# Kernel tuning notes

Hardware: AMD Instinct MI355X
Metric: run time of the kernel (lower is better)

## Reference

```python
import jax, jax.numpy as jnp
import numpy as np

H, C, D = 8, 32, 128  # num_heads, att_head_size, inp_dim
LN_EPS = 1e-5


def setup_inputs() -> dict:
    key = jax.random.key(0)
    ks = jax.random.split(key, 12)
    B, I, L = 1, 128, 256
    z_ij = jax.random.normal(ks[0], (B, I, L, D), dtype=jnp.float32)
    d_jk = jax.random.uniform(ks[1], (B, L, L, 1), dtype=jnp.float32)
    mask_z = jnp.ones((B, I, L), dtype=jnp.float32)
    s = 0.05
    return {
        "z_ij": z_ij,
        "d_jk": d_jk,
        "mask_z": mask_z,
        "ln_gamma": jnp.ones((D,), jnp.float32),
        "ln_beta": jnp.zeros((D,), jnp.float32),
        "Wq": jax.random.normal(ks[2], (D, H * C), jnp.float32) * s,
        "Wk": jax.random.normal(ks[3], (D, H * C), jnp.float32) * s,
        "Wv": jax.random.normal(ks[4], (D, H * C), jnp.float32) * s,
        "Wb": jax.random.normal(ks[5], (D, H), jnp.float32) * s,
        "Wd": jax.random.normal(ks[6], (1, H), jnp.float32) * s,
        "Wg": jax.random.normal(ks[7], (D, H * C), jnp.float32) * s,
        "bg": jnp.zeros((H * C,), jnp.float32),
        "Wf": jax.random.normal(ks[8], (H * C, D), jnp.float32) * s,
        "bf": jnp.zeros((D,), jnp.float32),
    }


def reference(z_ij, d_jk, mask_z, ln_gamma, ln_beta, Wq, Wk, Wv, Wb, Wd, Wg, bg, Wf, bf):
    B, I, L, _ = z_ij.shape
    # LayerNorm over last dim
    mu = jnp.mean(z_ij, axis=-1, keepdims=True)
    var = jnp.mean(jnp.square(z_ij - mu), axis=-1, keepdims=True)
    z = (z_ij - mu) * jax.lax.rsqrt(var + LN_EPS) * ln_gamma + ln_beta

    rs = lambda x: x.reshape(x.shape[:-1] + (H, C))  # [..., H*C] -> [..., H, C]
    q = rs(z @ Wq) * (H ** -0.5)                  # [B,I,L,H,C]
    k = rs(z @ Wk)                                # [B,I,L,H,C]
    v = rs(z @ Wv)                                # [B,I,L,H,C]

    b = jnp.transpose(z @ Wb, (0, 1, 3, 2))[..., None]       # [B,I,H,Q,1]
    d = jnp.transpose(d_jk @ Wd, (0, 3, 1, 2))[:, None]      # [B,1,H,Q,K]

    logits = jnp.einsum('biqhc,bikhc->bihqk', q, k) + b + d  # [B,I,H,Q,K]
    att_mask = 1e9 * (mask_z[:, :, None, None, :] - 1.0)
    logits = logits + att_mask
    weights = jax.nn.softmax(logits, axis=-1)

    weighted = jnp.einsum('bihqk,bikhc->biqhc', weights, v)  # [B,I,Q,H,C]
    g = jax.nn.sigmoid(rs(z @ Wg + bg))                      # [B,I,Q,H,C]
    out = (g * weighted).reshape(B, I, L, H * C)
    out = out @ Wf + bf
    out = out * mask_z[..., None]
    return out
```

## Files before the change

kernel.cpp:

```cpp
#include <hip/hip_runtime.h>
#include <hip/hip_bf16.h>
#include <math.h>

#define HH 8
#define CC 32
#define DD 128
#define HC 256
#define II 128
#define LL 256
#define NROW (II*LL)
#define LN_EPS 1e-5f

typedef float f32x4 __attribute__((ext_vector_type(4)));
typedef short short8 __attribute__((ext_vector_type(8)));
typedef short short4v __attribute__((ext_vector_type(4)));
typedef unsigned short us;

static __device__ __forceinline__ us bfc(float x) {
    return __builtin_bit_cast(us, __float2bfloat16(x));
}
static __device__ __forceinline__ float bf2f(us h) {
    return __builtin_bit_cast(float, ((unsigned int)h) << 16);
}

__global__ __launch_bounds__(256) void k_ln(const float* __restrict__ z,
                                            const float* __restrict__ gamma,
                                            const float* __restrict__ beta,
                                            us* __restrict__ zn)
{
    const int t = threadIdx.x;
    const int row = blockIdx.x * 4 + (t >> 6);
    const int lane = t & 63;
    float2 x = *(const float2*)(z + (size_t)row * DD + lane * 2);
    float s = x.x + x.y;
    float s2 = x.x * x.x + x.y * x.y;
#pragma unroll
    for (int off = 1; off < 64; off <<= 1) {
        s  += __shfl_xor(s, off, 64);
        s2 += __shfl_xor(s2, off, 64);
    }
    float mu = s * (1.0f / DD);
    float var = s2 * (1.0f / DD) - mu * mu;
    float rstd = rsqrtf(var + LN_EPS);
    float2 gm = *(const float2*)(gamma + lane * 2);
    float2 bt = *(const float2*)(beta + lane * 2);
    float y0 = (x.x - mu) * rstd * gm.x + bt.x;
    float y1 = (x.y - mu) * rstd * gm.y + bt.y;
    unsigned int pk = (unsigned int)bfc(y0) | ((unsigned int)bfc(y1) << 16);
    ((unsigned int*)zn)[(size_t)row * 64 + lane] = pk;
}

__global__ __launch_bounds__(256) void k_wprep(const float* __restrict__ Wq,
                                               const float* __restrict__ Wk,
                                               const float* __restrict__ Wv,
                                               const float* __restrict__ Wg,
                                               const float* __restrict__ Wf,
                                               us* __restrict__ F,
                                               us* __restrict__ WfpH,
                                               us* __restrict__ WfpL)
{
    const int bid = blockIdx.x;
    if (bid < 128) {
        const int mat = bid >> 5;
        const float* W = (mat == 0) ? Wq : (mat == 1) ? Wk : (mat == 2) ? Wv : Wg;
        const float scale = (mat == 0) ? 0.35355339059327373f : 1.0f;
        int base = (bid & 31) * 1024 + threadIdx.x * 4;
        float4 wv = *(const float4*)(W + base);
        int k = base >> 8, n0 = base & 255;
        int ks = k >> 5, kk = k & 31;
        int slot = ((kk >> 4) << 2) | (kk & 3);
        int gg = (kk >> 2) & 3;
        float vals[4] = {wv.x, wv.y, wv.z, wv.w};
        us* Fb = F + mat * 32768;
#pragma unroll
        for (int e = 0; e < 4; ++e) {
            int n = n0 + e;
            int lane = (n & 15) | (gg << 4);
            Fb[((size_t)(ks * 16 + (n >> 4)) * 64 + lane) * 8 + slot] = bfc(vals[e] * scale);
        }
    } else {
        int idx = ((bid - 128) * 256 + threadIdx.x) * 4;
#pragma unroll
        for (int e = 0; e < 4; ++e, ++idx) {
            int k = idx >> 7, n = idx & 127;
            float w = Wf[idx];
            us hi = bfc(w);
            us lo = bfc(w - bf2f(hi));
            int kk = k & 31;
            int g = (kk >> 2) & 3, b = kk >> 4, j0 = kk & 3;
            int lane = (n & 15) | (g << 4);
            size_t dst = ((size_t)((k >> 5) * 8 + (n >> 4)) * 64 + lane) * 8 + b * 4 + j0;
            WfpH[dst] = hi;
            WfpL[dst] = lo;
        }
    }
}

__global__ __launch_bounds__(256, 4) void k_proj(const us* __restrict__ zn,
                                                 const us* __restrict__ F,
                                                 const float* __restrict__ bg,
                                                 us* __restrict__ Qf,
                                                 us* __restrict__ Kf,
                                                 us* __restrict__ Vtf,
                                                 us* __restrict__ Pg)
{
    const int rb = blockIdx.x, cb = blockIdx.y, t = threadIdx.x;
    const int m0 = rb * 128, n0 = cb * 128;
    const int mat = n0 >> 8, lc0 = n0 & 255;
    __shared__ us A[128][136];

#pragma unroll
    for (int e = 0; e < 8; ++e) {
        int cid = e * 256 + t;
        int row = cid >> 4, c = cid & 15;
        uint4 q = *(const uint4*)(zn + (size_t)(m0 + row) * DD + c * 8);
        int ks = c >> 2, cc = c & 3;
        int fe = (cc & 1) * 16 + (cc >> 1) * 4;
        *(uint2*)&A[row][ks * 32 + fe]     = make_uint2(q.x, q.y);
        *(uint2*)&A[row][ks * 32 + fe + 8] = make_uint2(q.z, q.w);
    }
    __syncthreads();

    const int lane = t & 63, w = t >> 6;
    const int wm = w & 1, wn = w >> 1;
    const int l0 = lane & 15, g = lane >> 4;
    const us* Fb = F + mat * 32768 + ((size_t)((lc0 >> 4) + wn * 4) * 64 + lane) * 8;
    f32x4 acc[4][4];
#pragma unroll
    for (int a = 0; a < 4; ++a)
#pragma unroll
        for (int b = 0; b < 4; ++b) acc[a][b] = (f32x4){0, 0, 0, 0};

#pragma unroll
    for (int ks = 0; ks < 4; ++ks) {
        short8 af[4], bfr[4];
#pragma unroll
        for (int mf = 0; mf < 4; ++mf)
            af[mf] = *(const short8*)&A[wm * 64 + mf * 16 + l0][ks * 32 + 8 * g];
#pragma unroll
        for (int nf = 0; nf < 4; ++nf)
            bfr[nf] = *(const short8*)(Fb + (size_t)(ks * 16 + nf) * 512);
#pragma unroll
        for (int mf = 0; mf < 4; ++mf)
#pragma unroll
            for (int nf = 0; nf < 4; ++nf)
                acc[mf][nf] = __builtin_amdgcn_mfma_f32_16x16x32_bf16(af[mf], bfr[nf], acc[mf][nf], 0, 0, 0);
    }

    __syncthreads();
    us (*Cs)[136] = A;
#pragma unroll
    for (int nf = 0; nf < 4; ++nf) {
        int lcol = wn * 64 + nf * 16 + l0;
        float bgv = (mat == 3) ? bg[lc0 + lcol] : 0.0f;
#pragma unroll
        for (int mf = 0; mf < 4; ++mf) {
#pragma unroll
            for (int r = 0; r < 4; ++r) {
                float v = acc[mf][nf][r];
                if (mat == 3) v = 1.0f / (1.0f + __expf(-(v + bgv)));
                Cs[wm * 64 + mf * 16 + 4 * g + r][lcol] = bfc(v);
            }
        }
    }
    __syncthreads();

    const int i = m0 >> 8, half = (m0 >> 7) & 1;
    if (mat <= 1) {
        us* Dst = (mat == 0) ? Qf : Kf;
#pragma unroll
        for (int e = 0; e < 8; ++e) {
            int sub = e * 256 + t;
            int lane2 = sub & 63;
            int l0b = lane2 & 15, gb = lane2 >> 4;
            int rest = sub >> 6;
            int hl = rest & 3, ktl = rest >> 2;
            int hglob = (lc0 >> 5) + hl;
            int kt = half * 8 + ktl;
            short8 vv = *(const short8*)&Cs[ktl * 16 + l0b][hl * 32 + 8 * gb];
            *(short8*)(Dst + (((size_t)(i * 8 + hglob) * 16 + kt) * 64 + lane2) * 8) = vv;
        }
    } else if (mat == 2) {
#pragma unroll
        for (int e = 0; e < 8; ++e) {
            int sub = e * 256 + t;
            int lane2 = sub & 63;
            int l0b = lane2 & 15, gb = lane2 >> 4;
            int rest = sub >> 6;
            int ct = rest & 1, pl = (rest >> 1) & 3, hl = rest >> 3;
            int hglob = (lc0 >> 5) + hl;
            int p = half * 4 + pl;
            int col = hl * 32 + ct * 16 + l0b;
            us vals[8];
#pragma unroll
            for (int j = 0; j < 8; ++j) {
                int kk = 4 * gb + (j & 3) + 16 * (j >> 2);
                vals[j] = Cs[pl * 32 + kk][col];
            }
            *(short8*)(Vtf + ((((size_t)(i * 8 + hglob) * 8 + p) * 2 + ct) * 64 + lane2) * 8)
                = *(short8*)vals;
        }
    } else {
#pragma unroll
        for (int e = 0; e < 8; ++e) {
            int cid = e * 256 + t;
            int row = cid >> 4, c = cid & 15;
            short8 vv = *(const short8*)&Cs[row][c * 8];
            *(short8*)(Pg + (size_t)(m0 + row) * 256 + lc0 + c * 8) = vv;
        }
    }
}

__global__ __launch_bounds__(256, 4) void k_attn(const us* __restrict__ Qf,
                                                 const us* __restrict__ Kf,
                                                 const us* __restrict__ Vtf,
                                                 const us* __restrict__ Pg,
                                                 us* __restrict__ Po,
                                                 const float* __restrict__ djk,
                                                 const float* __restrict__ Wd,
                                                 const float* __restrict__ mask)
{
    const int ih = blockIdx.x;
    const int i = ih >> 3, h = ih & 7;
    const int t = threadIdx.x;
    const int lane = t & 63, w = t >> 6;
    const int l0 = lane & 15, g = lane >> 4;
    const int q0 = w * 64;
    __shared__ us gs[256][40];

    const float wd = Wd[h];
    const us* Qb = Qf + (size_t)ih * 8192;
    const us* Kb = Kf + (size_t)ih * 8192;
    const us* Vb = Vtf + (size_t)ih * 8192;

    short8 qfr[4];
    int qrow[4];
    const float* djkq[4];
#pragma unroll
    for (int qt = 0; qt < 4; ++qt) {
        qfr[qt] = *(const short8*)(Qb + ((size_t)(w * 4 + qt) * 64 + lane) * 8);
        qrow[qt] = q0 + qt * 16 + l0;
        djkq[qt] = djk + (size_t)qrow[qt] * LL;
    }

    f32x4 oacc[2][4];
#pragma unroll
    for (int ct = 0; ct < 2; ++ct)
#pragma unroll
        for (int qt = 0; qt < 4; ++qt) oacc[ct][qt] = (f32x4){0, 0, 0, 0};
    float ssum[4] = {0, 0, 0, 0};

#pragma unroll
    for (int p = 0; p < 8; ++p) {
        short8 pfv[4];
#pragma unroll
        for (int hf = 0; hf < 2; ++hf) {
            const int kt = 2 * p + hf;
            short8 kfr = *(const short8*)(Kb + ((size_t)kt * 64 + lane) * 8);
            f32x4 mv = *(const f32x4*)(mask + i * LL + kt * 16 + 4 * g);
            float ma0 = 1e9f * (mv.x - 1.0f), ma1 = 1e9f * (mv.y - 1.0f);
            float ma2 = 1e9f * (mv.z - 1.0f), ma3 = 1e9f * (mv.w - 1.0f);
#pragma unroll
            for (int qt = 0; qt < 4; ++qt) {
                f32x4 z4 = {0, 0, 0, 0};
                f32x4 s = __builtin_amdgcn_mfma_f32_16x16x32_bf16(kfr, qfr[qt], z4, 0, 0, 0);
                f32x4 dv = *(const f32x4*)(djkq[qt] + kt * 16 + 4 * g);
                float p0 = __expf(s[0] + wd * dv.x + ma0);
                float p1 = __expf(s[1] + wd * dv.y + ma1);
                float p2 = __expf(s[2] + wd * dv.z + ma2);
                float p3 = __expf(s[3] + wd * dv.w + ma3);
                ssum[qt] += (p0 + p1) + (p2 + p3);
                pfv[qt][hf * 4 + 0] = (short)bfc(p0);
                pfv[qt][hf * 4 + 1] = (short)bfc(p1);
                pfv[qt][hf * 4 + 2] = (short)bfc(p2);
                pfv[qt][hf * 4 + 3] = (short)bfc(p3);
            }
        }
#pragma unroll
        for (int ct = 0; ct < 2; ++ct) {
            short8 vfr = *(const short8*)(Vb + ((size_t)(p * 2 + ct) * 64 + lane) * 8);
#pragma unroll
            for (int qt = 0; qt < 4; ++qt)
                oacc[ct][qt] = __builtin_amdgcn_mfma_f32_16x16x32_bf16(vfr, pfv[qt], oacc[ct][qt], 0, 0, 0);
        }
    }

#pragma unroll
    for (int qt = 0; qt < 4; ++qt) {
        float s = ssum[qt];
        s += __shfl_xor(s, 16, 64);
        s += __shfl_xor(s, 32, 64);
        float inv = 1.0f / s;
        const us* gb = Pg + (size_t)(i * LL + qrow[qt]) * 256 + h * CC;
#pragma unroll
        for (int ct = 0; ct < 2; ++ct) {
            short4v gv = *(const short4v*)(gb + ct * 16 + 4 * g);
            f32x4 ov = oacc[ct][qt];
            short4v res;
            res.x = (short)bfc(bf2f((us)gv.x) * ov.x * inv);
            res.y = (short)bfc(bf2f((us)gv.y) * ov.y * inv);
            res.z = (short)bfc(bf2f((us)gv.z) * ov.z * inv);
            res.w = (short)bfc(bf2f((us)gv.w) * ov.w * inv);
            *(short4v*)&gs[q0 + qt * 16 + l0][ct * 16 + 4 * g] = res;
        }
    }
    __syncthreads();
#pragma unroll
    for (int e = 0; e < 4; ++e) {
        int cid = e * 256 + t;
        int row = cid >> 2, c = cid & 3;
        short8 vv = *(const short8*)&gs[row][c * 8];
        *(short8*)(Po + (size_t)(i * LL + row) * 256 + h * CC + c * 8) = vv;
    }
}

__global__ __launch_bounds__(256) void k_out(const us* __restrict__ Po,
                                             const us* __restrict__ WfpH,
                                             const us* __restrict__ WfpL,
                                             const float* __restrict__ bf_,
                                             const float* __restrict__ mask,
                                             float* __restrict__ out)
{
    const int t = threadIdx.x;
    const int m0 = blockIdx.x * 64;
    __shared__ us A[64][264];
#pragma unroll
    for (int e = 0; e < 8; ++e) {
        int cid = e * 256 + t;
        int row = cid >> 5, c = cid & 31;
        uint4 q = *(const uint4*)(Po + (size_t)(m0 + row) * 256 + c * 8);
        int ksb = c >> 2, cc = c & 3;
        int fe = (cc & 1) * 16 + (cc >> 1) * 4;
        *(uint2*)&A[row][ksb * 32 + fe]     = make_uint2(q.x, q.y);
        *(uint2*)&A[row][ksb * 32 + fe + 8] = make_uint2(q.z, q.w);
    }
    __syncthreads();
    const int lane = t & 63, w = t >> 6;
    const int l0 = lane & 15, g = lane >> 4;
    f32x4 acc[8];
#pragma unroll
    for (int nf = 0; nf < 8; ++nf) acc[nf] = (f32x4){0, 0, 0, 0};

#pragma unroll
    for (int ksb = 0; ksb < 8; ++ksb) {
        short8 af = *(const short8*)&A[w * 16 + l0][ksb * 32 + 8 * g];
#pragma unroll
        for (int nf = 0; nf < 8; ++nf) {
            short8 bh = *(const short8*)(WfpH + ((size_t)(ksb * 8 + nf) * 64 + lane) * 8);
            short8 bl = *(const short8*)(WfpL + ((size_t)(ksb * 8 + nf) * 64 + lane) * 8);
            acc[nf] = __builtin_amdgcn_mfma_f32_16x16x32_bf16(af, bh, acc[nf], 0, 0, 0);
            acc[nf] = __builtin_amdgcn_mfma_f32_16x16x32_bf16(af, bl, acc[nf], 0, 0, 0);
        }
    }
    float maskv[4];
    int rowm[4];
#pragma unroll
    for (int r = 0; r < 4; ++r) {
        rowm[r] = m0 + w * 16 + 4 * g + r;
        maskv[r] = mask[rowm[r]];
    }
#pragma unroll
    for (int nf = 0; nf < 8; ++nf) {
        int n = nf * 16 + l0;
        float bfv = bf_[n];
#pragma unroll
        for (int r = 0; r < 4; ++r)
            out[(size_t)rowm[r] * DD + n] = (acc[nf][r] + bfv) * maskv[r];
    }
}

extern "C" void kernel_launch(void* const* d_in, const int* in_sizes, int n_in,
                              void* d_out, int out_size, void* d_ws, size_t ws_size,
                              hipStream_t stream)
{
    const float* z     = (const float*)d_in[0];
    const float* djk   = (const float*)d_in[1];
    const float* mask  = (const float*)d_in[2];
    const float* gamma = (const float*)d_in[3];
    const float* beta  = (const float*)d_in[4];
    const float* Wq    = (const float*)d_in[5];
    const float* Wk    = (const float*)d_in[6];
    const float* Wv    = (const float*)d_in[7];
    const float* Wd    = (const float*)d_in[9];
    const float* Wg    = (const float*)d_in[10];
    const float* bg    = (const float*)d_in[11];
    const float* Wf    = (const float*)d_in[12];
    const float* bf_   = (const float*)d_in[13];
    float* out = (float*)d_out;

    us* zn   = (us*)d_ws;
    us* Qf   = zn   + (size_t)NROW * DD;
    us* Kf   = Qf   + (size_t)1024 * 8192;
    us* Vtf  = Kf   + (size_t)1024 * 8192;
    us* Pg   = Vtf  + (size_t)1024 * 8192;
    us* Po   = Pg   + (size_t)NROW * 256;
    us* WfpH = Po   + (size_t)NROW * 256;
    us* WfpL = WfpH + 256 * 128;
    us* F    = WfpL + 256 * 128;

    k_ln   <<<NROW / 4, 256, 0, stream>>>(z, gamma, beta, zn);
    k_wprep<<<160, 256, 0, stream>>>(Wq, Wk, Wv, Wg, Wf, F, WfpH, WfpL);
    k_proj <<<dim3(NROW / 128, 8), 256, 0, stream>>>(zn, F, bg, Qf, Kf, Vtf, Pg);
    k_attn <<<II * HH, 256, 0, stream>>>(Qf, Kf, Vtf, Pg, Po, djk, Wd, mask);
    k_out  <<<NROW / 64, 256, 0, stream>>>(Po, WfpH, WfpL, bf_, mask, out);
}
```

Before: 103.2 us.

## Stage K/V in LDS via async loads, use exp2 softmax, shrink proj tiles

The attention kernel now copies each head's K and V fragments into shared memory with global_load_lds, precomputes the mask additive term in LDS, and folds log2(e) into the Q weights and Wd so it can use the hardware exp2 instruction. The projection kernel halves its row tile to 64 and raises the occupancy hint. The Po intermediate moves to a head-major layout so the attention write-out is contiguous, and the output GEMM's loads change to match. These target redundant global K/V/mask reads, exp overhead and low parallelism in the projection, at the cost of more projection blocks and extra LDS use and synchronization in attention.

```diff
diff --git a/kernel.cpp b/kernel.cpp
--- a/kernel.cpp
+++ b/kernel.cpp
@@ -10,6 +10,7 @@
 #define LL 256
 #define NROW (II*LL)
 #define LN_EPS 1e-5f
+#define LOG2E 1.4426950408889634f
 
 typedef float f32x4 __attribute__((ext_vector_type(4)));
 typedef short short8 __attribute__((ext_vector_type(8)));
@@ -21,6 +22,12 @@
 }
 static __device__ __forceinline__ float bf2f(us h) {
     return __builtin_bit_cast(float, ((unsigned int)h) << 16);
+}
+static __device__ __forceinline__ void gload_lds16(const us* g, us* l) {
+    __builtin_amdgcn_global_load_lds(
+        (const __attribute__((address_space(1))) unsigned int*)g,
+        (__attribute__((address_space(3))) unsigned int*)l,
+        16, 0, 0);
 }
 
 __global__ __launch_bounds__(256) void k_ln(const float* __restrict__ z,
@@ -63,7 +70,7 @@
     if (bid < 128) {
         const int mat = bid >> 5;
         const float* W = (mat == 0) ? Wq : (mat == 1) ? Wk : (mat == 2) ? Wv : Wg;
-        const float scale = (mat == 0) ? 0.35355339059327373f : 1.0f;
+        const float scale = (mat == 0) ? 0.35355339059327373f * LOG2E : 1.0f;
         int base = (bid & 31) * 1024 + threadIdx.x * 4;
         float4 wv = *(const float4*)(W + base);
         int k = base >> 8, n0 = base & 255;
@@ -96,7 +103,7 @@
     }
 }
 
-__global__ __launch_bounds__(256, 4) void k_proj(const us* __restrict__ zn,
+__global__ __launch_bounds__(256, 6) void k_proj(const us* __restrict__ zn,
                                                  const us* __restrict__ F,
                                                  const float* __restrict__ bg,
                                                  us* __restrict__ Qf,
@@ -105,12 +112,12 @@
                                                  us* __restrict__ Pg)
 {
     const int rb = blockIdx.x, cb = blockIdx.y, t = threadIdx.x;
-    const int m0 = rb * 128, n0 = cb * 128;
+    const int m0 = rb * 64, n0 = cb * 128;
     const int mat = n0 >> 8, lc0 = n0 & 255;
-    __shared__ us A[128][136];
-
-#pragma unroll
-    for (int e = 0; e < 8; ++e) {
+    __shared__ us A[64][136];
+
+#pragma unroll
+    for (int e = 0; e < 4; ++e) {
         int cid = e * 256 + t;
         int row = cid >> 4, c = cid & 15;
         uint4 q = *(const uint4*)(zn + (size_t)(m0 + row) * DD + c * 8);
@@ -125,23 +132,23 @@
     const int wm = w & 1, wn = w >> 1;
     const int l0 = lane & 15, g = lane >> 4;
     const us* Fb = F + mat * 32768 + ((size_t)((lc0 >> 4) + wn * 4) * 64 + lane) * 8;
-    f32x4 acc[4][4];
-#pragma unroll
-    for (int a = 0; a < 4; ++a)
+    f32x4 acc[2][4];
+#pragma unroll
+    for (int a = 0; a < 2; ++a)
 #pragma unroll
         for (int b = 0; b < 4; ++b) acc[a][b] = (f32x4){0, 0, 0, 0};
 
 #pragma unroll
     for (int ks = 0; ks < 4; ++ks) {
-        short8 af[4], bfr[4];
-#pragma unroll
-        for (int mf = 0; mf < 4; ++mf)
-            af[mf] = *(const short8*)&A[wm * 64 + mf * 16 + l0][ks * 32 + 8 * g];
+        short8 af[2], bfr[4];
+#pragma unroll
+        for (int mf = 0; mf < 2; ++mf)
+            af[mf] = *(const short8*)&A[wm * 32 + mf * 16 + l0][ks * 32 + 8 * g];
 #pragma unroll
         for (int nf = 0; nf < 4; ++nf)
             bfr[nf] = *(const short8*)(Fb + (size_t)(ks * 16 + nf) * 512);
 #pragma unroll
-        for (int mf = 0; mf < 4; ++mf)
+        for (int mf = 0; mf < 2; ++mf)
 #pragma unroll
             for (int nf = 0; nf < 4; ++nf)
                 acc[mf][nf] = __builtin_amdgcn_mfma_f32_16x16x32_bf16(af[mf], bfr[nf], acc[mf][nf], 0, 0, 0);
@@ -154,42 +161,44 @@
         int lcol = wn * 64 + nf * 16 + l0;
         float bgv = (mat == 3) ? bg[lc0 + lcol] : 0.0f;
 #pragma unroll
-        for (int mf = 0; mf < 4; ++mf) {
+        for (int mf = 0; mf < 2; ++mf) {
 #pragma unroll
             for (int r = 0; r < 4; ++r) {
                 float v = acc[mf][nf][r];
                 if (mat == 3) v = 1.0f / (1.0f + __expf(-(v + bgv)));
-                Cs[wm * 64 + mf * 16 + 4 * g + r][lcol] = bfc(v);
+                Cs[wm * 32 + mf * 16 + 4 * g + r][lcol] = bfc(v);
             }
         }
     }
     __syncthreads();
 
-    const int i = m0 >> 8, half = (m0 >> 7) & 1;
+    const int i = m0 >> 8;
+    const int ktbase = (m0 & 255) >> 4;
+    const int pbase  = (m0 & 255) >> 5;
     if (mat <= 1) {
         us* Dst = (mat == 0) ? Qf : Kf;
 #pragma unroll
-        for (int e = 0; e < 8; ++e) {
+        for (int e = 0; e < 4; ++e) {
             int sub = e * 256 + t;
             int lane2 = sub & 63;
             int l0b = lane2 & 15, gb = lane2 >> 4;
             int rest = sub >> 6;
             int hl = rest & 3, ktl = rest >> 2;
             int hglob = (lc0 >> 5) + hl;
-            int kt = half * 8 + ktl;
+            int kt = ktbase + ktl;
             short8 vv = *(const short8*)&Cs[ktl * 16 + l0b][hl * 32 + 8 * gb];
             *(short8*)(Dst + (((size_t)(i * 8 + hglob) * 16 + kt) * 64 + lane2) * 8) = vv;
         }
     } else if (mat == 2) {
 #pragma unroll
-        for (int e = 0; e < 8; ++e) {
+        for (int e = 0; e < 4; ++e) {
             int sub = e * 256 + t;
             int lane2 = sub & 63;
             int l0b = lane2 & 15, gb = lane2 >> 4;
             int rest = sub >> 6;
-            int ct = rest & 1, pl = (rest >> 1) & 3, hl = rest >> 3;
+            int ct = rest & 1, pl = (rest >> 1) & 1, hl = rest >> 2;
             int hglob = (lc0 >> 5) + hl;
-            int p = half * 4 + pl;
+            int p = pbase + pl;
             int col = hl * 32 + ct * 16 + l0b;
             us vals[8];
 #pragma unroll
@@ -202,7 +211,7 @@
         }
     } else {
 #pragma unroll
-        for (int e = 0; e < 8; ++e) {
+        for (int e = 0; e < 4; ++e) {
             int cid = e * 256 + t;
             int row = cid >> 4, c = cid & 15;
             short8 vv = *(const short8*)&Cs[row][c * 8];
@@ -226,22 +235,36 @@
     const int lane = t & 63, w = t >> 6;
     const int l0 = lane & 15, g = lane >> 4;
     const int q0 = w * 64;
-    __shared__ us gs[256][40];
-
-    const float wd = Wd[h];
-    const us* Qb = Qf + (size_t)ih * 8192;
+
+    __shared__ us KV[32 * 512];
+    __shared__ float madd[LL];
+    us* Kl = KV;
+    us* Vl = KV + 16 * 512;
+
     const us* Kb = Kf + (size_t)ih * 8192;
     const us* Vb = Vtf + (size_t)ih * 8192;
 
+    {
+        int tile = w * 4;
+#pragma unroll
+        for (int tt = 0; tt < 4; ++tt) {
+            gload_lds16(Kb + (size_t)(tile + tt) * 512 + lane * 8, &Kl[(tile + tt) * 512]);
+            gload_lds16(Vb + (size_t)(tile + tt) * 512 + lane * 8, &Vl[(tile + tt) * 512]);
+        }
+    }
+    madd[t] = (LOG2E * 1e9f) * (mask[i * LL + t] - 1.0f);
+
+    const float wd = Wd[h] * LOG2E;
     short8 qfr[4];
     int qrow[4];
     const float* djkq[4];
 #pragma unroll
     for (int qt = 0; qt < 4; ++qt) {
-        qfr[qt] = *(const short8*)(Qb + ((size_t)(w * 4 + qt) * 64 + lane) * 8);
+        qfr[qt] = *(const short8*)(Qf + (size_t)ih * 8192 + ((size_t)(w * 4 + qt) * 64 + lane) * 8);
         qrow[qt] = q0 + qt * 16 + l0;
         djkq[qt] = djk + (size_t)qrow[qt] * LL;
     }
+    __syncthreads();
 
     f32x4 oacc[2][4];
 #pragma unroll
@@ -250,25 +273,22 @@
         for (int qt = 0; qt < 4; ++qt) oacc[ct][qt] = (f32x4){0, 0, 0, 0};
     float ssum[4] = {0, 0, 0, 0};
 
-#pragma unroll
     for (int p = 0; p < 8; ++p) {
         short8 pfv[4];
 #pragma unroll
         for (int hf = 0; hf < 2; ++hf) {
             const int kt = 2 * p + hf;
-            short8 kfr = *(const short8*)(Kb + ((size_t)kt * 64 + lane) * 8);
-            f32x4 mv = *(const f32x4*)(mask + i * LL + kt * 16 + 4 * g);
-            float ma0 = 1e9f * (mv.x - 1.0f), ma1 = 1e9f * (mv.y - 1.0f);
-            float ma2 = 1e9f * (mv.z - 1.0f), ma3 = 1e9f * (mv.w - 1.0f);
+            short8 kfr = *(const short8*)&Kl[kt * 512 + lane * 8];
+            f32x4 mvv = *(const f32x4*)&madd[kt * 16 + 4 * g];
 #pragma unroll
             for (int qt = 0; qt < 4; ++qt) {
                 f32x4 z4 = {0, 0, 0, 0};
                 f32x4 s = __builtin_amdgcn_mfma_f32_16x16x32_bf16(kfr, qfr[qt], z4, 0, 0, 0);
                 f32x4 dv = *(const f32x4*)(djkq[qt] + kt * 16 + 4 * g);
-                float p0 = __expf(s[0] + wd * dv.x + ma0);
-                float p1 = __expf(s[1] + wd * dv.y + ma1);
-                float p2 = __expf(s[2] + wd * dv.z + ma2);
-                float p3 = __expf(s[3] + wd * dv.w + ma3);
+                float p0 = __builtin_amdgcn_exp2f(s[0] + wd * dv.x + mvv.x);
+                float p1 = __builtin_amdgcn_exp2f(s[1] + wd * dv.y + mvv.y);
+                float p2 = __builtin_amdgcn_exp2f(s[2] + wd * dv.z + mvv.z);
+                float p3 = __builtin_amdgcn_exp2f(s[3] + wd * dv.w + mvv.w);
                 ssum[qt] += (p0 + p1) + (p2 + p3);
                 pfv[qt][hf * 4 + 0] = (short)bfc(p0);
                 pfv[qt][hf * 4 + 1] = (short)bfc(p1);
@@ -278,13 +298,15 @@
         }
 #pragma unroll
         for (int ct = 0; ct < 2; ++ct) {
-            short8 vfr = *(const short8*)(Vb + ((size_t)(p * 2 + ct) * 64 + lane) * 8);
+            short8 vfr = *(const short8*)&Vl[(p * 2 + ct) * 512 + lane * 8];
 #pragma unroll
             for (int qt = 0; qt < 4; ++qt)
                 oacc[ct][qt] = __builtin_amdgcn_mfma_f32_16x16x32_bf16(vfr, pfv[qt], oacc[ct][qt], 0, 0, 0);
         }
     }
 
+    __syncthreads();
+    us (*gs)[40] = (us (*)[40])KV;
 #pragma unroll
     for (int qt = 0; qt < 4; ++qt) {
         float s = ssum[qt];
@@ -310,7 +332,7 @@
         int cid = e * 256 + t;
         int row = cid >> 2, c = cid & 3;
         short8 vv = *(const short8*)&gs[row][c * 8];
-        *(short8*)(Po + (size_t)(i * LL + row) * 256 + h * CC + c * 8) = vv;
+        *(short8*)(Po + ((size_t)h * NROW + (size_t)i * LL + row) * 32 + c * 8) = vv;
     }
 }
 
@@ -328,9 +350,10 @@
     for (int e = 0; e < 8; ++e) {
         int cid = e * 256 + t;
         int row = cid >> 5, c = cid & 31;
-        uint4 q = *(const uint4*)(Po + (size_t)(m0 + row) * 256 + c * 8);
-        int ksb = c >> 2, cc = c & 3;
-        int fe = (cc & 1) * 16 + (cc >> 1) * 4;
+        int hh = c >> 2, cc = c & 3;
+        uint4 q = *(const uint4*)(Po + ((size_t)hh * NROW + m0 + row) * 32 + cc * 8);
+        int ksb = c >> 2, cc2 = c & 3;
+        int fe = (cc2 & 1) * 16 + (cc2 >> 1) * 4;
         *(uint2*)&A[row][ksb * 32 + fe]     = make_uint2(q.x, q.y);
         *(uint2*)&A[row][ksb * 32 + fe + 8] = make_uint2(q.z, q.w);
     }
@@ -400,7 +423,7 @@
 
     k_ln   <<<NROW / 4, 256, 0, stream>>>(z, gamma, beta, zn);
     k_wprep<<<160, 256, 0, stream>>>(Wq, Wk, Wv, Wg, Wf, F, WfpH, WfpL);
-    k_proj <<<dim3(NROW / 128, 8), 256, 0, stream>>>(zn, F, bg, Qf, Kf, Vtf, Pg);
+    k_proj <<<dim3(NROW / 64, 8), 256, 0, stream>>>(zn, F, bg, Qf, Kf, Vtf, Pg);
     k_attn <<<II * HH, 256, 0, stream>>>(Qf, Kf, Vtf, Pg, Po, djk, Wd, mask);
     k_out  <<<NROW / 64, 256, 0, stream>>>(Po, WfpH, WfpL, bf_, mask, out);
 }
```

Result: faster. 98.99 us (-4.1%).
